# Optimization experiments

Hardware: AMD Instinct MI355X
Metric: run time of the kernel (lower is better)

Reference implementation:

```python
import jax, jax.numpy as jnp
import numpy as np

B, S, V, E, HL = 64, 30, 5000, 300, 256
TWOH = 2 * HL
KB, MAPD, MEMD, MLP, NCLS = 512, 512, 512, 1024, 32
L, T, NMOD, NOPS = 8, 9, 9, 6
IH, IW, CIN = 15, 10, 512 + 128


def setup_inputs():
    key = jax.random.key(0)
    ks = iter(jax.random.split(key, 64))
    g = lambda shape, s=0.05: jax.random.normal(next(ks), shape, jnp.float32) * s
    inp = {}
    inp['image'] = g((B, CIN, IH, IW), 1.0)
    inp['ques'] = jax.random.randint(next(ks), (B, S), 0, V)
    ql = jnp.sort(jax.random.randint(next(ks), (B,), 1, S + 1))[::-1]
    inp['q_len'] = ql.at[0].set(S)
    inp['embed_W'] = g((V, E))
    for d in ('f', 'b'):
        inp['lstm_Wi_' + d] = g((E, 4 * HL))
        inp['lstm_Wh_' + d] = g((HL, 4 * HL))
        inp['lstm_b_' + d] = jnp.zeros((4 * HL,), jnp.float32)
    inp['W1'] = g((T, TWOH, TWOH))
    inp['b_1'] = jnp.zeros((TWOH,), jnp.float32)
    inp['W2_w'] = g((2 * TWOH, TWOH)); inp['W2_b'] = jnp.zeros((TWOH,), jnp.float32)
    inp['W3'] = g((TWOH,))
    inp['c_0'] = g((TWOH,), 1.0)
    inp['Wmod'] = g((TWOH, NMOD))
    inp['ic1_w'] = g((KB, CIN)); inp['ic1_b'] = g((KB,), 1.0)
    inp['ic2_w'] = g((KB, KB)); inp['ic2_b'] = g((KB,), 1.0)
    inp['i2m_w'] = g((MAPD, KB)); inp['i2m_b'] = g((MAPD,), 1.0)
    inp['t2m_w'] = g((TWOH, MAPD)); inp['t2m_b'] = jnp.zeros((MAPD,), jnp.float32)
    inp['cell3_ow'] = g((4, NOPS), 1.0)
    inp['cell3_cw'] = g((4, MAPD)); inp['cell3_cb'] = jnp.zeros((4,), jnp.float32)
    inp['cell4_ow'] = g((2, NOPS), 1.0)
    inp['cell4_cw'] = g((2, MAPD)); inp['cell4_cb'] = jnp.zeros((2,), jnp.float32)
    inp['ans_ow'] = g((2, NOPS), 1.0)
    inp['ans_W'] = g((2, 2 * MAPD, MEMD)); inp['ans_b'] = jnp.zeros((2, MEMD), jnp.float32)
    inp['out1_w'] = g((TWOH + MEMD, MLP)); inp['out1_b'] = jnp.zeros((MLP,), jnp.float32)
    inp['out2_w'] = g((MLP, NCLS)); inp['out2_b'] = jnp.zeros((NCLS,), jnp.float32)
    return inp


def _conv1x1(x, w, b):
    return jnp.einsum('bchw,oc->bohw', x, w) + b[None, :, None, None]


def _lstm_dir(xW, Wh, mask, reverse):
    # xW: [S,B,4H], mask: [S,B,1] ; torch LSTM gate order i,f,g,o
    Bn, Hn = xW.shape[1], Wh.shape[0]
    def step(carry, inp):
        h, c = carry
        xw, m = inp
        z = xw + h @ Wh
        i, f, gg, o = jnp.split(z, 4, axis=-1)
        cn = jax.nn.sigmoid(f) * c + jax.nn.sigmoid(i) * jnp.tanh(gg)
        hn = jax.nn.sigmoid(o) * jnp.tanh(cn)
        return (jnp.where(m, hn, h), jnp.where(m, cn, c)), jnp.where(m, hn, 0.0)
    init = (jnp.zeros((Bn, Hn), xW.dtype), jnp.zeros((Bn, Hn), xW.dtype))
    (hF, _), outs = jax.lax.scan(step, init, (xW, mask), reverse=reverse)
    return hF, outs


def _mix3(ow, x, a, t):
    # soft op mixing (DARTS-style) for 3-input cells: x [B,D,H,W], a [B,H,W], t [B,D]
    w = jax.nn.softmax(ow)
    a4 = a[:, None]; t4 = t[:, :, None, None]
    ops = (x * t4, x + t4, x * a4, x * t4 * a4, x, a4 * t4)
    return jax.nn.elu(sum(w[k] * ops[k] for k in range(NOPS)))


def _mix4(ow, x, a1, a2, t):
    w = jax.nn.softmax(ow)
    a14 = a1[:, None]; a24 = a2[:, None]; t4 = t[:, :, None, None]
    ops = (x * t4, x + t4, x * a14, x * a24, x * a14 * a24, x * t4 * (a14 + a24))
    return jax.nn.elu(sum(w[k] * ops[k] for k in range(NOPS)))


def _forward(image, ques, q_len, embed_W, lstm_Wi_f, lstm_Wh_f, lstm_b_f, lstm_Wi_b, lstm_Wh_b, lstm_b_b, W1, b_1, W2_w, W2_b, W3, c_0, Wmod, ic1_w, ic1_b, ic2_w, ic2_b, i2m_w, i2m_b, t2m_w, t2m_b, cell3_ow, cell3_cw, cell3_cb, cell4_ow, cell4_cw, cell4_cb, ans_ow, ans_W, ans_b, out1_w, out1_b, out2_w, out2_b):
    # img_conv (1x1 conv -> ELU -> 1x1 conv)
    x = jax.nn.elu(_conv1x1(image, ic1_w, ic1_b))
    x = _conv1x1(x, ic2_w, ic2_b)
    Bn, _, Hh, Ww = x.shape
    Sn = ques.shape[1]
    # bi-LSTM over the (packed, i.e. masked) question
    emb = embed_W[ques]                                   # [B,S,E]
    mask = (jnp.arange(Sn)[None, :] < q_len[:, None])     # [B,S]
    mT = mask.T[:, :, None].astype(x.dtype) > 0           # [S,B,1] bool
    xWf = (emb @ lstm_Wi_f + lstm_b_f).transpose(1, 0, 2)
    xWb = (emb @ lstm_Wi_b + lstm_b_b).transpose(1, 0, 2)
    hF, oF = _lstm_dir(xWf, lstm_Wh_f, mT, False)
    hB, oB = _lstm_dir(xWb, lstm_Wh_b, mT, True)
    lstm_out = jnp.concatenate([oF, oB], -1).transpose(1, 0, 2)  # [B,S,2H], zero at pads
    q = jnp.concatenate([hF, hB], -1)                            # [B,2H]
    img_map = _conv1x1(x, i2m_w, i2m_b)                          # [B,MAP,H,W]
    stack = jnp.zeros((Bn, Hh, Ww, L), x.dtype)
    p = jnp.zeros((Bn, L), x.dtype).at[:, 0].set(1.0)
    mem = jnp.zeros((Bn, MEMD), x.dtype)
    c_prev = jnp.tile(c_0[None], (Bn, 1))
    e0 = jnp.zeros((L,), x.dtype).at[0].set(1.0)
    imp_loss = jnp.float32(0.0)
    read = lambda st, pp: jnp.einsum('bhwl,bl->bhw', st, pp)
    dec = lambda pp: jnp.concatenate([pp[:, 1:], jnp.zeros_like(pp[:, :1])], 1) + pp * e0
    for t in range(T):
        u = jnp.concatenate([q @ W1[t] + b_1, c_prev], 1) @ W2_w + W2_b  # [B,2H]
        wl = u @ Wmod                                                     # [B,9]
        ls = jax.nn.log_softmax(wl, axis=1)
        imp_loss = imp_loss - jnp.sum(jnp.exp(ls) * ls)
        w = jnp.exp(ls)
        attn = jax.nn.softmax(jnp.einsum('bsh,h->bs', lstm_out * u[:, None, :], W3), axis=1)
        c = jnp.einsum('bs,bsh->bh', attn, lstm_out)
        c_prev = c
        tmap = c @ t2m_w + t2m_b
        stacks, ps = [], []
        a_top = read(stack, p)     # attention at stack top
        # modules 0-3: overwrite at current pointer (pointer shift is commented out in source)
        for m in range(4):
            out = jnp.einsum('bdhw,d->bhw', _mix3(cell3_ow[m], img_map, a_top, tmap), cell3_cw[m]) + cell3_cb[m]
            pb = p[:, None, None, :]
            stacks.append(stack * (1.0 - pb) + out[..., None] * pb)
            ps.append(p)
        # modules 4-5: pop one (soft pointer decrement), then write
        p_dec = dec(p)
        a2 = read(stack, p_dec)
        for m in range(2):
            out = jnp.einsum('bdhw,d->bhw', _mix4(cell4_ow[m], img_map, a_top, a2, tmap), cell4_cw[m]) + cell4_cb[m]
            pb = p_dec[:, None, None, :]
            stacks.append(stack * (1.0 - pb) + out[..., None] * pb)
            ps.append(p_dec)
        # modules 6-7: answer cells -> memory update, stack untouched
        pooled6 = jnp.mean(_mix3(ans_ow[0], img_map, a_top, tmap), axis=(2, 3))
        mem6 = jnp.concatenate([pooled6, tmap], 1) @ ans_W[0] + ans_b[0]
        stacks.append(stack); ps.append(p)
        pooled7 = jnp.mean(_mix4(ans_ow[1], img_map, a_top, a2, tmap), axis=(2, 3))
        mem7 = jnp.concatenate([pooled7, tmap], 1) @ ans_W[1] + ans_b[1]
        stacks.append(stack); ps.append(p_dec)
        # module 8: NoOp
        stacks.append(stack); ps.append(p)
        # soft mixing over modules (the scatter-heavy part)
        stack = jnp.einsum('bm,bmhwl->bhwl', w, jnp.stack(stacks, 1))
        p = jnp.einsum('bm,bml->bl', w, jnp.stack(ps, 1))
        mem = w[:, 6:7] * mem6 + w[:, 7:8] * mem7 + (1.0 - w[:, 6:7] - w[:, 7:8]) * mem
    h1 = jax.nn.elu(jnp.concatenate([q, mem], 1) @ out1_w + out1_b)
    logits = h1 @ out2_w + out2_b
    return logits, imp_loss


def reference(image, ques, q_len, embed_W, lstm_Wi_f, lstm_Wh_f, lstm_b_f, lstm_Wi_b, lstm_Wh_b, lstm_b_b, W1, b_1, W2_w, W2_b, W3, c_0, Wmod, ic1_w, ic1_b, ic2_w, ic2_b, i2m_w, i2m_b, t2m_w, t2m_b, cell3_ow, cell3_cw, cell3_cb, cell4_ow, cell4_cw, cell4_cb, ans_ow, ans_W, ans_b, out1_w, out1_b, out2_w, out2_b):
    return _forward(image, ques, q_len, embed_W, lstm_Wi_f, lstm_Wh_f, lstm_b_f, lstm_Wi_b, lstm_Wh_b, lstm_b_b, W1, b_1, W2_w, W2_b, W3, c_0, Wmod, ic1_w, ic1_b, ic2_w, ic2_b, i2m_w, i2m_b, t2m_w, t2m_b, cell3_ow, cell3_cw, cell3_cb, cell4_ow, cell4_cw, cell4_cb, ans_ow, ans_W, ans_b, out1_w, out1_b, out2_w, out2_b)
```

## Files before the change

kernel.cpp:

```cpp
#include <hip/hip_runtime.h>
#include <hip/hip_fp16.h>
#include <math.h>

#define DEV __device__ __forceinline__

DEV float fexp(float x){ return __expf(x); }
DEV float elu_(float x){ return x > 0.f ? x : fexp(x) - 1.f; }
DEV float sigm_(float x){ return 1.f/(1.f + fexp(-x)); }
DEV float tanh_(float x){ float e = fexp(2.f*x); return 1.f - 2.f/(e + 1.f); }
DEV unsigned bf16r(float x){ unsigned u = __float_as_uint(x);
  return (u + 0x7fffu + ((u>>16)&1u)) >> 16; }
DEV float blo(unsigned u){ return __uint_as_float(u << 16); }
DEV float bhi(unsigned u){ return __uint_as_float(u & 0xffff0000u); }
DEV float bl(unsigned short u){ return __uint_as_float(((unsigned)u) << 16); }

using frag  = __attribute__((ext_vector_type(8))) short;
using fragh = __attribute__((ext_vector_type(8))) _Float16;
using f32x4 = __attribute__((ext_vector_type(4))) float;

DEV uint4 cload16w(const void* p){
  uint4 r;
  asm volatile("global_load_dwordx4 %0, %1, off sc0 sc1\n\ts_waitcnt vmcnt(0)"
               : "=v"(r) : "v"(p) : "memory");
  return r;
}
DEV uint4 cload16nw(const void* p){
  uint4 r;
  asm volatile("global_load_dwordx4 %0, %1, off sc0 sc1"
               : "=v"(r) : "v"(p) : "memory");
  return r;
}

DEV void d_packB(const float* __restrict__ W, short* __restrict__ Bp,
                 int KC, int Ng, int Ksrc, int N, int trans, int idx)
{
  if (idx >= KC*Ng*64) return;
  int lane = idx & 63;
  int g    = (idx >> 6) % Ng;
  int kc   = idx / (64*Ng);
  int n = g*16 + (lane & 15);
  int kb = kc*32 + ((lane >> 4) << 3);
  unsigned o[4];
#pragma unroll
  for (int jj = 0; jj < 4; ++jj) {
    int k0 = kb + 2*jj;
    float v0 = (k0   < Ksrc) ? (trans ? W[(size_t)n*Ksrc + k0]   : W[(size_t)(k0)*N + n])   : 0.f;
    float v1 = (k0+1 < Ksrc) ? (trans ? W[(size_t)n*Ksrc + k0+1] : W[(size_t)(k0+1)*N + n]) : 0.f;
    o[jj] = bf16r(v0) | (bf16r(v1) << 16);
  }
  *(uint4*)(Bp + (size_t)idx*8) = make_uint4(o[0], o[1], o[2], o[3]);
}

DEV void d_packImg(const float* __restrict__ image, short* __restrict__ Ap, int idx)
{
  int lane = idx & 63;
  int kc   = (idx >> 6) % 20;
  int mt   = idx / 1280;
  int row = mt*16 + (lane & 15);
  int b = row / 150, p = row % 150;
  int cb = kc*32 + ((lane >> 4) << 3);
  unsigned o[4];
#pragma unroll
  for (int jj = 0; jj < 4; ++jj) {
    float v0 = image[((size_t)b*640 + cb + 2*jj    )*150 + p];
    float v1 = image[((size_t)b*640 + cb + 2*jj + 1)*150 + p];
    o[jj] = bf16r(v0) | (bf16r(v1) << 16);
  }
  *(uint4*)(Ap + (size_t)idx*8) = make_uint4(o[0], o[1], o[2], o[3]);
}

DEV void d_packEmb(const float* __restrict__ embedW, const int* __restrict__ ques,
                   short* __restrict__ Ap, int idx)
{
  int lane = idx & 63;
  int kc   = (idx >> 6) % 10;
  int mt   = idx / 640;
  int row = mt*16 + (lane & 15);
  int q = ques[row];
  int kb = kc*32 + ((lane >> 4) << 3);
  unsigned o[4];
#pragma unroll
  for (int jj = 0; jj < 4; ++jj) {
    int k0 = kb + 2*jj;
    float v0 = (k0   < 300) ? embedW[(size_t)q*300 + k0]   : 0.f;
    float v1 = (k0+1 < 300) ? embedW[(size_t)q*300 + k0+1] : 0.f;
    o[jj] = bf16r(v0) | (bf16r(v1) << 16);
  }
  *(uint4*)(Ap + (size_t)idx*8) = make_uint4(o[0], o[1], o[2], o[3]);
}

__global__ __launch_bounds__(256)
void megapack_k(const float* __restrict__ c0, const float* __restrict__ c3ow,
                const float* __restrict__ c4ow, const float* __restrict__ aow,
                float* __restrict__ stack, float* __restrict__ pvecA,
                float* __restrict__ mem, float* __restrict__ cprev,
                float* __restrict__ swb, float* __restrict__ pl,
                const float* __restrict__ Whf, const float* __restrict__ Whb,
                unsigned* __restrict__ whT,
                float* __restrict__ hbufz, int* __restrict__ flagz,
                const float* __restrict__ ic1w, short* __restrict__ w1p,
                const float* __restrict__ ic2w, short* __restrict__ w2mp,
                const float* __restrict__ i2mw, short* __restrict__ w3mp,
                const float* __restrict__ Wif, short* __restrict__ wifp,
                const float* __restrict__ Wib, short* __restrict__ wibp,
                const float* __restrict__ image, short* __restrict__ imgP,
                const float* __restrict__ embedW, const int* __restrict__ ques,
                short* __restrict__ embp,
                const float* __restrict__ t2mw, unsigned* __restrict__ t2pp,
                const float* __restrict__ W2w, unsigned short* __restrict__ w2bp,
                const float* __restrict__ ansW, unsigned short* __restrict__ answp)
{
  const int bx = blockIdx.x, tid = threadIdx.x;
  if (bx < 320) {
    int idx = bx*256 + tid;
    int stride = 320*256;
    for (int i = idx; i < 64*150*8; i += stride) stack[i] = 0.f;
    for (int i = idx; i < 64*8;    i += stride) pvecA[i] = ((i & 7) == 0) ? 1.f : 0.f;
    for (int i = idx; i < 64*512;  i += stride) mem[i] = 0.f;
    for (int i = idx; i < 64*512;  i += stride) cprev[i] = c0[i & 511];
    for (int i = idx; i < 9*2*64*512; i += stride) pl[i] = 0.f;
    for (int i = idx; i < 32768;   i += stride) hbufz[i] = 0.f;
    if (idx < 256) flagz[idx] = 0;
    if (idx < 8) {
      const float* ow = (idx < 4) ? (c3ow + idx*6)
                      : (idx < 6) ? (c4ow + (idx-4)*6)
                                  : (aow  + (idx-6)*6);
      float mx = ow[0];
      for (int m = 1; m < 6; ++m) mx = fmaxf(mx, ow[m]);
      float e[6]; float s = 0.f;
      for (int m = 0; m < 6; ++m) { e[m] = fexp(ow[m]-mx); s += e[m]; }
      for (int m = 0; m < 6; ++m) swb[idx*6+m] = e[m]/s;
    }
  } else if (bx < 1344) {
    int idx = (bx-320)*256 + tid;
    int dd  = idx >> 17;
    int rem = idx & 131071;
    int kp  = rem >> 10;
    int zc  = rem & 1023;
    const float* Wh = dd ? Whb : Whf;
    __half2 hv = __floats2half2_rn(Wh[(size_t)(2*kp)*1024 + zc],
                                   Wh[(size_t)(2*kp+1)*1024 + zc]);
    whT[((size_t)dd << 17) + (zc << 7) + kp] = *(unsigned*)&hv;
  } else if (bx < 1504) {
    d_packB(ic1w, w1p, 20, 32, 640, 512, 1, (bx-1344)*256 + tid);
  } else if (bx < 1632) {
    d_packB(ic2w, w2mp, 16, 32, 512, 512, 1, (bx-1504)*256 + tid);
  } else if (bx < 1760) {
    d_packB(i2mw, w3mp, 16, 32, 512, 512, 1, (bx-1632)*256 + tid);
  } else if (bx < 1920) {
    d_packB(Wif, wifp, 10, 64, 300, 1024, 0, (bx-1760)*256 + tid);
  } else if (bx < 2080) {
    d_packB(Wib, wibp, 10, 64, 300, 1024, 0, (bx-1920)*256 + tid);
  } else if (bx < 5080) {
    d_packImg(image, imgP, (bx-2080)*256 + tid);
  } else if (bx < 5380) {
    d_packEmb(embedW, ques, embp, (bx-5080)*256 + tid);
  } else if (bx < 5892) {
    int idx = (bx-5380)*256 + tid;
    int k = idx >> 8, c = idx & 255;
    t2pp[idx] = bf16r(t2mw[(size_t)k*512 + c]) | (bf16r(t2mw[(size_t)k*512 + 256 + c]) << 16);
  } else if (bx < 7940) {
    int i = (bx-5892)*256 + tid;
    w2bp[i] = (unsigned short)bf16r(W2w[i]);
  } else {
    int i = (bx-7940)*256 + tid;
    answp[i] = (unsigned short)bf16r(ansW[i]);
  }
}

__global__ __launch_bounds__(256)
void gemmM_k(const short* __restrict__ ApA, const short* __restrict__ ApB,
             const short* __restrict__ BpA, const short* __restrict__ BpB,
             const float* __restrict__ biasA, const float* __restrict__ biasB,
             void* __restrict__ CoutA, void* __restrict__ CoutB,
             int KC, int Ng, int N, int mode, int act, int KCout)
{
  __shared__ float lds[4][16][68];
  const int z = blockIdx.z;
  const short* Ap = z ? ApB : ApA;
  const short* Bp = z ? BpB : BpA;
  const float* bias = z ? biasB : biasA;
  void* Cout = z ? CoutB : CoutA;
  const int tid = threadIdx.x, lane = tid & 63, w = tid >> 6;
// ... 145 lines not shown
              const float* __restrict__ c1bias, short* __restrict__ c1out)
{
  const int tid = threadIdx.x, lane = tid & 63, w = tid >> 6;
  __shared__ union {
    unsigned short Wl[65536];
    float lds[4][16][68];
  } sm;

  if (blockIdx.x >= 32) {
    const int bx2 = (int)blockIdx.x - 32;
    const int mt = (bx2 >> 3)*4 + w;
    const int ncol0 = (bx2 & 7)*64;
    const short* Abase = c1Ap + (((size_t)mt*20) << 9) + lane*8;
    const short* Bbase = c1Bp + (((size_t)(bx2 & 7)*4) << 9) + lane*8;
    f32x4 acc0 = {0.f,0.f,0.f,0.f}, acc1 = acc0, acc2 = acc0, acc3 = acc0;
#pragma unroll 2
    for (int kc = 0; kc < 20; ++kc) {
      frag a = *(const frag*)(Abase + ((size_t)kc << 9));
      const short* bk = Bbase + (((size_t)kc*32) << 9);
      frag b0 = *(const frag*)(bk);
      frag b1 = *(const frag*)(bk + 512);
      frag b2 = *(const frag*)(bk + 1024);
      frag b3 = *(const frag*)(bk + 1536);
      acc0 = __builtin_amdgcn_mfma_f32_16x16x32_bf16(a, b0, acc0, 0, 0, 0);
      acc1 = __builtin_amdgcn_mfma_f32_16x16x32_bf16(a, b1, acc1, 0, 0, 0);
      acc2 = __builtin_amdgcn_mfma_f32_16x16x32_bf16(a, b2, acc2, 0, 0, 0);
      acc3 = __builtin_amdgcn_mfma_f32_16x16x32_bf16(a, b3, acc3, 0, 0, 0);
    }
    {
      int colb = lane & 15, rowb = (lane >> 4)*4;
#pragma unroll
      for (int r = 0; r < 4; ++r) {
        sm.lds[w][rowb+r][ 0+colb] = acc0[r];
        sm.lds[w][rowb+r][16+colb] = acc1[r];
        sm.lds[w][rowb+r][32+colb] = acc2[r];
        sm.lds[w][rowb+r][48+colb] = acc3[r];
      }
    }
    __syncthreads();
    {
      int m = lane & 15, qb = (lane >> 4)*8;
#pragma unroll
      for (int h = 0; h < 2; ++h) {
        int nl = h*32 + qb;
        unsigned o[4];
#pragma unroll
        for (int jj = 0; jj < 4; ++jj) {
          float v0 = elu_(sm.lds[w][m][nl + 2*jj]     + c1bias[ncol0 + nl + 2*jj]);
          float v1 = elu_(sm.lds[w][m][nl + 2*jj + 1] + c1bias[ncol0 + nl + 2*jj + 1]);
          o[jj] = bf16r(v0) | (bf16r(v1) << 16);
        }
        *(uint4*)(c1out + (((size_t)mt*16 + (ncol0 >> 5) + h) << 9) + lane*8)
            = make_uint4(o[0], o[1], o[2], o[3]);
      }
    }
    return;
  }

  const int bx = blockIdx.x;
  const int d = bx & 1, g = (bx >> 1) & 3, n = bx >> 3;
  const int q = lane >> 4, cl = lane & 15;

#pragma unroll 4
  for (int rb = 0; rb < 32; ++rb) {
    int lcrow = rb*8 + (tid >> 5);
    int gt = lcrow >> 6, c = lcrow & 63;
    int zc = gt*256 + n*64 + c;
    uint4 v = *(const uint4*)(whT + (((size_t)d*1024 + zc) << 7) + ((tid & 31) << 2));
    int byteoff = (lcrow << 9) + ((((tid & 31) << 4)) ^ ((lcrow & 7) << 4));
    *(uint4*)((char*)sm.Wl + byteoff) = v;
  }

  const float* xW = d ? xWb : xWf;
  const int b   = g*16 + cl;
  const int c4  = w*16 + q*4;
  const int hc4 = n*64 + c4;
  const int len = qlen[b];
  float cst[4] = {0.f,0.f,0.f,0.f}, hst[4] = {0.f,0.f,0.f,0.f};
  int* flg = flags + ((d*4 + g) << 2);
  const int bofs = (cl & 7) << 4;
  __syncthreads();

  for (int ss = 0; ss < 30; ++ss) {
    const int s = d ? (29 - ss) : ss;
    const float* xr = xW + (size_t)b*30720 + (size_t)s*1024 + hc4;
    f32x4 xwv[4];
#pragma unroll
    for (int gt = 0; gt < 4; ++gt) xwv[gt] = *(const f32x4*)(xr + gt*256);

    if (ss > 0) {
      for (;;) {
        uint4 f4 = cload16w(flg);
        if ((int)f4.x >= ss && (int)f4.y >= ss &&
            (int)f4.z >= ss && (int)f4.w >= ss) break;
      }
      __builtin_amdgcn_sched_barrier(0);
    }
    const char* hbr = (const char*)(hbuf + ((size_t)(((ss & 1)*2 + d)*4 + g) << 9))
                    + (cl << 9) + (q << 4);
    union { uint4 u; fragh f; } hv[8];
#pragma unroll
    for (int ks = 0; ks < 8; ++ks) hv[ks].u = cload16nw(hbr + (ks << 6));
    asm volatile("s_waitcnt vmcnt(0)" ::: "memory");
    __builtin_amdgcn_sched_barrier(0);

    f32x4 acc0 = {0.f,0.f,0.f,0.f}, acc1 = acc0, acc2 = acc0, acc3 = acc0;
#pragma unroll
    for (int ks = 0; ks < 8; ++ks) {
      const int kb = ((ks << 6) + (q << 4)) ^ bofs;
      const char* wb = (const char*)sm.Wl + ((w*16 + cl) << 9) + kb;
      fragh a0 = *(const fragh*)(wb);
      fragh a1 = *(const fragh*)(wb + (64 << 9));
      fragh a2 = *(const fragh*)(wb + (128 << 9));
      fragh a3 = *(const fragh*)(wb + (192 << 9));
      acc0 = __builtin_amdgcn_mfma_f32_16x16x32_f16(a0, hv[ks].f, acc0, 0, 0, 0);
      acc1 = __builtin_amdgcn_mfma_f32_16x16x32_f16(a1, hv[ks].f, acc1, 0, 0, 0);
      acc2 = __builtin_amdgcn_mfma_f32_16x16x32_f16(a2, hv[ks].f, acc2, 0, 0, 0);
      acc3 = __builtin_amdgcn_mfma_f32_16x16x32_f16(a3, hv[ks].f, acc3, 0, 0, 0);
    }
    const bool m = s < len;
    f32x4 lo4;
    float hvv[4];
#pragma unroll
    for (int r = 0; r < 4; ++r) {
      float iv = acc0[r] + xwv[0][r];
      float fv = acc1[r] + xwv[1][r];
      float gv = acc2[r] + xwv[2][r];
      float o_ = acc3[r] + xwv[3][r];
      float cn = sigm_(fv)*cst[r] + sigm_(iv)*tanh_(gv);
      float hn = sigm_(o_)*tanh_(cn);
      float hk = m ? hn : hst[r];
      cst[r] = m ? cn : cst[r];
      hst[r] = hk;
      hvv[r] = hk;
      lo4[r] = m ? hn : 0.f;
    }
    unsigned long long* hbw = hbuf + ((size_t)((((ss & 1) ^ 1)*2 + d)*4 + g) << 9);
    union { unsigned long long u; __half2 h2[2]; } hp;
    hp.h2[0] = __floats2half2_rn(hvv[0], hvv[1]);
    hp.h2[1] = __floats2half2_rn(hvv[2], hvv[3]);
    __hip_atomic_store(hbw + cl*64 + (hc4 >> 2), hp.u,
                       __ATOMIC_RELAXED, __HIP_MEMORY_SCOPE_AGENT);
    *(f32x4*)(lstm_out + (((size_t)b*30 + s) << 9) + (d << 8) + hc4) = lo4;
    asm volatile("s_waitcnt vmcnt(0)" ::: "memory");
    __syncthreads();
    if (tid == 0)
      __hip_atomic_store(&flg[n], ss + 1, __ATOMIC_RELAXED, __HIP_MEMORY_SCOPE_AGENT);
  }
  *(f32x4*)(qout + ((size_t)b << 9) + (d << 8) + hc4) =
      f32x4{hst[0], hst[1], hst[2], hst[3]};
}

__global__ __launch_bounds__(1024)
void kcattn3_k(const float* __restrict__ u, const float* __restrict__ Wmod,
               const float* __restrict__ lstm_out, const float* __restrict__ W3,
               const unsigned* __restrict__ t2pp, const float* __restrict__ t2mb,
               float* __restrict__ woutAll, float* __restrict__ imp_part,
               float* __restrict__ cout, float* __restrict__ tmapv, int t)
{
  int b = blockIdx.x;
  int tid = threadIdx.x;
  int lane = tid & 63, wave = tid >> 6;
  __shared__ float ush[512];
  __shared__ float sC[512];
  __shared__ float cpart[512];
  __shared__ float tpart[4][512];
  __shared__ float wl[9];
  __shared__ float sc[32], at[32];
  if (tid < 512) ush[tid] = u[b*512 + tid];
  __syncthreads();
  for (int s = wave; s < 30; s += 16) {
    float acc = 0.f;
    const float* lo = lstm_out + ((size_t)b*30 + s)*512;
#pragma unroll
    for (int h = lane; h < 512; h += 64) acc += lo[h]*ush[h]*W3[h];
#pragma unroll
    for (int off = 32; off; off >>= 1) acc += __shfl_down(acc, off);
    if (lane == 0) sc[s] = acc;
  }
  if (wave < 9) {
    float acc = 0.f;
#pragma unroll
    for (int k = lane; k < 512; k += 64) acc += ush[k]*Wmod[k*9+wave];
#pragma unroll
    for (int off = 32; off; off >>= 1) acc += __shfl_down(acc, off);
    if (lane == 0) wl[wave] = acc;
  }
  __syncthreads();
  if (tid == 0) {
    float mx = wl[0];
    for (int m = 1; m < 9; ++m) mx = fmaxf(mx, wl[m]);
    float s = 0.f;
    for (int m = 0; m < 9; ++m) s += fexp(wl[m]-mx);
    float ls = logf(s);
    float ent = 0.f;
    for (int m = 0; m < 9; ++m) {
      float l = wl[m]-mx-ls;
      float w = fexp(l);
      woutAll[t*576 + b*9 + m] = w;
      ent -= w*l;
    }
    imp_part[t*64+b] = ent;
  }
  if (wave == 1) {
    float v = (lane < 30) ? sc[lane] : -3.4e38f;
    float mx = v;
#pragma unroll
    for (int off = 32; off; off >>= 1) mx = fmaxf(mx, __shfl_xor(mx, off));
    float e = (lane < 30) ? fexp(v-mx) : 0.f;
    float ssum = e;
#pragma unroll
    for (int off = 32; off; off >>= 1) ssum += __shfl_xor(ssum, off);
    if (lane < 30) at[lane] = e/ssum;
  }
  __syncthreads();
  {
    int h = tid & 511, seg = tid >> 9;
    float acc = 0.f;
    int s0 = seg ? 15 : 0, s1 = seg ? 30 : 15;
    for (int s = s0; s < s1; ++s) acc += at[s]*lstm_out[((size_t)b*30 + s)*512 + h];
    if (seg) cpart[h] = acc;
    __syncthreads();
    if (!seg) {
      float tot = acc + cpart[h];
      cout[b*512+h] = tot;
      sC[h] = tot;
    }
  }
  __syncthreads();
  {
    int c2 = tid & 255, ks = tid >> 8;
    float a0 = 0.f, a1 = 0.f;
    const unsigned* tp = t2pp + c2;
#pragma unroll 8
    for (int k = ks*128; k < ks*128 + 128; ++k) {
      float cv = sC[k];
      unsigned wv2 = tp[(size_t)k*256];
      a0 += cv*blo(wv2);
      a1 += cv*bhi(wv2);
    }
    tpart[ks][c2]       = a0;
    tpart[ks][256 + c2] = a1;
  }
  __syncthreads();
  if (tid < 512) {
    float v = tpart[0][tid] + tpart[1][tid] + tpart[2][tid] + tpart[3][tid];
    tmapv[b*512 + tid] = v + t2mb[tid];
  }
}

__global__ __launch_bounds__(256)
void modu_k(const unsigned short* __restrict__ imapB, const float* __restrict__ tmapv,
            float* __restrict__ stack, const float* __restrict__ pvecIn,
            float* __restrict__ pvecOut,
            const float* __restrict__ swb, const float* __restrict__ c3w,
            const float* __restrict__ c3b, const float* __restrict__ c4w,
            const float* __restrict__ c4b, const float* __restrict__ wmod,
            float* __restrict__ plt,
            const float* __restrict__ tmp1n, const float* __restrict__ cprevB,
            const unsigned short* __restrict__ w2bp, const float* __restrict__ W2b,
            float* __restrict__ ubuf, int do_u)
{
  __shared__ union {
    struct { float sT[512]; float pv[8], pd[8], wm[9]; float wpart[4][2][512]; } m;
    struct { __align__(16) float As[8][1024]; float part[4][8][64]; } u;
  } sm;
  int pb = blockIdx.y;
  int lane = threadIdx.x & 63, wave = threadIdx.x >> 6;
  if (pb == 19) {
    if (!do_u) return;
    const int x = blockIdx.x;
    const int r0 = (x >> 3) * 8, nc0 = (x & 7) * 64;
    for (int e4 = threadIdx.x; e4 < 2048; e4 += 256) {
      int r = e4 >> 8;
      int k4 = (e4 & 255) << 2;
      float4 v = (k4 < 512)
          ? *(const float4*)&tmp1n [(size_t)(r0+r)*512 + k4]
          : *(const float4*)&cprevB[(size_t)(r0+r)*512 + (k4 - 512)];
      *(float4*)&sm.u.As[r][k4] = v;
    }
    __syncthreads();
    const int k0 = wave * 256;
    const unsigned short* Bp = w2bp + (size_t)k0*512 + nc0 + lane;
    float acc[8] = {0,0,0,0,0,0,0,0};
#pragma unroll 4
    for (int kk = 0; kk < 256; ++kk) {
      float bv = bl(Bp[(size_t)kk*512]);
#pragma unroll
      for (int r = 0; r < 8; ++r) acc[r] += sm.u.As[r][k0+kk] * bv;
    }
#pragma unroll
    for (int r = 0; r < 8; ++r) sm.u.part[wave][r][lane] = acc[r];
    __syncthreads();
    {
      int r = threadIdx.x >> 6, c = lane;
#pragma unroll
      for (int p2 = 0; p2 < 2; ++p2) {
        int rr = r + p2*4;
        float s2 = sm.u.part[0][rr][c] + sm.u.part[1][rr][c]
                 + sm.u.part[2][rr][c] + sm.u.part[3][rr][c];
        ubuf[(size_t)(r0 + rr)*512 + nc0 + c] = s2 + W2b[nc0 + c];
      }
    }
    return;
  }
  int b = blockIdx.x;
  for (int j = threadIdx.x; j < 512; j += 256) sm.m.sT[j] = tmapv[b*512 + j];
  if (threadIdx.x < 8) sm.m.pv[threadIdx.x] = pvecIn[b*8+threadIdx.x];
  if (threadIdx.x >= 64 && threadIdx.x < 73) sm.m.wm[threadIdx.x-64] = wmod[b*9 + threadIdx.x-64];
  __syncthreads();
  if (threadIdx.x < 8) {
    int l = threadIdx.x;
    sm.m.pd[l] = (l < 7 ? sm.m.pv[l+1] : 0.f) + (l == 0 ? sm.m.pv[0] : 0.f);
  }
  __syncthreads();
  if (pb == 0 && threadIdx.x < 8) {
    int l = threadIdx.x;
    float WP = sm.m.wm[0]+sm.m.wm[1]+sm.m.wm[2]+sm.m.wm[3] + sm.m.wm[6] + sm.m.wm[8];
    float WD = sm.m.wm[4]+sm.m.wm[5] + sm.m.wm[7];
    pvecOut[b*8+l] = WP*sm.m.pv[l] + WD*sm.m.pd[l];
  }

  float W[8][6];
#pragma unroll
  for (int m = 0; m < 8; ++m)
#pragma unroll
    for (int i = 0; i < 6; ++i) W[m][i] = swb[m*6+i];
  float W03 = sm.m.wm[0]+sm.m.wm[1]+sm.m.wm[2]+sm.m.wm[3];
  float W45 = sm.m.wm[4]+sm.m.wm[5];

  float acc6[8], acc7[8];
#pragma unroll
  for (int i = 0; i < 8; ++i) { acc6[i] = 0.f; acc7[i] = 0.f; }

  for (int pi = 0; pi < 2; ++pi) {
    int p = pb*8 + wave*2 + pi;
    if (p < 150) {
      const float* st = stack + ((size_t)b*150 + p)*8;
      float a = 0.f, av2 = 0.f;
#pragma unroll
      for (int l = 0; l < 8; ++l) { float v = st[l]; a += v*sm.m.pv[l]; av2 += v*sm.m.pd[l]; }
      float part[6] = {0,0,0,0,0,0};
#pragma unroll 2
      for (int i = 0; i < 8; ++i) {
        int d = i*64 + lane;
        float x = bl(imapB[((size_t)b*150 + p)*512 + d]);
        float t = sm.m.sT[d];
#pragma unroll
        for (int m = 0; m < 4; ++m) {
          float c1 = W[m][0]*t + W[m][1] + W[m][4] + (W[m][2] + W[m][3]*t)*a;
          float c0 = W[m][1]*t + W[m][5]*t*a;
          part[m] += elu_(c1*x + c0) * c3w[m*512+d];
        }
#pragma unroll
        for (int m = 0; m < 2; ++m) {
          float c1 = W[4+m][0]*t + W[4+m][1] + W[4+m][2]*a + W[4+m][3]*av2
                   + W[4+m][4]*a*av2 + W[4+m][5]*t*(a+av2);
          part[4+m] += elu_(c1*x + W[4+m][1]*t) * c4w[m*512+d];
        }
        float c16 = W[6][0]*t + W[6][1] + W[6][4] + (W[6][2] + W[6][3]*t)*a;
        float c06 = W[6][1]*t + W[6][5]*t*a;
        acc6[i] += elu_(c16*x + c06);
        float c17 = W[7][0]*t + W[7][1] + W[7][2]*a + W[7][3]*av2
                  + W[7][4]*a*av2 + W[7][5]*t*(a+av2);
        acc7[i] += elu_(c17*x + W[7][1]*t);
      }
#pragma unroll
      for (int m = 0; m < 6; ++m) {
#pragma unroll
        for (int off = 32; off; off >>= 1) part[m] += __shfl_down(part[m], off);
        part[m] = __shfl(part[m], 0);
      }
      float r3  = sm.m.wm[0]*(part[0]+c3b[0]) + sm.m.wm[1]*(part[1]+c3b[1])
                + sm.m.wm[2]*(part[2]+c3b[2]) + sm.m.wm[3]*(part[3]+c3b[3]);
      float r45 = sm.m.wm[4]*(part[4]+c4b[0]) + sm.m.wm[5]*(part[5]+c4b[1]);
      if (lane < 8) {
        int l = lane;
        size_t idx = ((size_t)b*150 + p)*8 + l;
        stack[idx] = stack[idx]*(1.f - W03*sm.m.pv[l] - W45*sm.m.pd[l])
                   + sm.m.pv[l]*r3 + sm.m.pd[l]*r45;
      }
    }
  }
#pragma unroll
  for (int i = 0; i < 8; ++i) {
    sm.m.wpart[wave][0][i*64+lane] = acc6[i];
    sm.m.wpart[wave][1][i*64+lane] = acc7[i];
  }
  __syncthreads();
  for (int e = threadIdx.x; e < 1024; e += 256) {
    int which = e >> 9, d = e & 511;
    float s = sm.m.wpart[0][which][d] + sm.m.wpart[1][which][d]
            + sm.m.wpart[2][which][d] + sm.m.wpart[3][which][d];
    atomicAdd(&plt[(size_t)which*32768 + b*512 + d], s * (1.f/150.f));
  }
}

__global__ __launch_bounds__(512)
void ansall_k(const float* __restrict__ plt, const float* __restrict__ tmapv,
              const unsigned short* __restrict__ answp, const float* __restrict__ ansb,
              float* __restrict__ m67o)
{
  const int z = blockIdx.z;
  const int t = z >> 1, zz = z & 1;
  __shared__ __align__(16) float As[8][1024];
  __shared__ float part[8][8][64];
  const int tid = threadIdx.x;
  const int r0 = blockIdx.y*8;
  const int nc0 = blockIdx.x*64;
  const int lane = tid & 63, w = tid >> 6;

  for (int e4 = tid; e4 < 1024; e4 += 512) {
    int r = e4 >> 7, k4 = (e4 & 127) << 2;
    *(float4*)&As[r][k4]     = *(const float4*)&plt[(size_t)z*32768 + (size_t)(r0+r)*512 + k4];
    *(float4*)&As[r][512+k4] = *(const float4*)&tmapv[(size_t)t*32768 + (size_t)(r0+r)*512 + k4];
  }
  __syncthreads();
  {
    const unsigned short* Bp = answp + (size_t)zz*524288
                             + (size_t)(w*128)*512 + nc0 + lane;
    float acc[8] = {0,0,0,0,0,0,0,0};
    int k0 = w*128;
#pragma unroll 8
    for (int kk = 0; kk < 128; ++kk) {
      float bv = bl(Bp[(size_t)kk*512]);
#pragma unroll
      for (int r = 0; r < 8; ++r) acc[r] += As[r][k0+kk]*bv;
    }
#pragma unroll
    for (int r = 0; r < 8; ++r) part[w][r][lane] = acc[r];
  }
  __syncthreads();
  {
    int r = tid >> 6, c = tid & 63;
    float s = 0.f;
#pragma unroll
    for (int w2 = 0; w2 < 8; ++w2) s += part[w2][r][c];
    m67o[(size_t)z*32768 + (size_t)(r0+r)*512 + nc0 + c] = s + ansb[zz*512 + nc0 + c];
  }
}

__global__ __launch_bounds__(512)
void memfin_k(const float* __restrict__ woutAll, const float* __restrict__ m67t,
              float* __restrict__ memb)
{
  int b = blockIdx.x;
  int tid = threadIdx.x;
  __shared__ float w6s[9], w7s[9], coef[9];
  if (tid < 9)       w6s[tid] = woutAll[tid*576 + b*9 + 6];
  else if (tid < 18) w7s[tid-9] = woutAll[(tid-9)*576 + b*9 + 7];
  __syncthreads();
  if (tid == 0) {
    float c = 1.f;
    for (int t = 8; t >= 0; --t) { coef[t] = c; c *= (1.f - w6s[t] - w7s[t]); }
  }
  __syncthreads();
  float acc = 0.f;
#pragma unroll
  for (int t = 0; t < 9; ++t) {
    float m6 = m67t[(((size_t)t*2 + 0)*64 + b)*512 + tid];
    float m7 = m67t[(((size_t)t*2 + 1)*64 + b)*512 + tid];
    acc += coef[t]*(w6s[t]*m6 + w7s[t]*m7);
  }
  memb[b*512 + tid] = acc;
}

__global__ __launch_bounds__(256)
void imp_k(const float* __restrict__ part, float* __restrict__ out)
{
  int lane = threadIdx.x & 63, wave = threadIdx.x >> 6;
  float acc = 0.f;
  for (int i = threadIdx.x; i < 576; i += 256) acc += part[i];
#pragma unroll
  for (int off = 32; off; off >>= 1) acc += __shfl_down(acc, off);
  __shared__ float red[4];
  if (lane == 0) red[wave] = acc;
  __syncthreads();
  if (threadIdx.x == 0) out[0] = red[0]+red[1]+red[2]+red[3];
}

extern "C" void kernel_launch(void* const* d_in, const int* in_sizes, int n_in,
                              void* d_out, int out_size, void* d_ws, size_t ws_size,
                              hipStream_t stream)
{
  (void)in_sizes; (void)n_in; (void)out_size; (void)ws_size;
  const float* image = (const float*)d_in[0];
  const int*   ques  = (const int*)d_in[1];
  const int*   qlen  = (const int*)d_in[2];
  const float* embedW= (const float*)d_in[3];
  const float* Wi_f  = (const float*)d_in[4];
  const float* Wh_f  = (const float*)d_in[5];
  const float* b_f   = (const float*)d_in[6];
  const float* Wi_b  = (const float*)d_in[7];
  const float* Wh_b  = (const float*)d_in[8];
  const float* b_b   = (const float*)d_in[9];
  const float* W1    = (const float*)d_in[10];
  const float* b1    = (const float*)d_in[11];
  const float* W2w   = (const float*)d_in[12];
  const float* W2b   = (const float*)d_in[13];
  const float* W3    = (const float*)d_in[14];
  const float* c0    = (const float*)d_in[15];
  const float* Wmod  = (const float*)d_in[16];
  const float* ic1w  = (const float*)d_in[17];
  const float* ic1b  = (const float*)d_in[18];
  const float* ic2w  = (const float*)d_in[19];
  const float* ic2b  = (const float*)d_in[20];
  const float* i2mw  = (const float*)d_in[21];
  const float* i2mb  = (const float*)d_in[22];
  const float* t2mw  = (const float*)d_in[23];
  const float* t2mb  = (const float*)d_in[24];
  const float* c3ow  = (const float*)d_in[25];
  const float* c3cw  = (const float*)d_in[26];
  const float* c3cb  = (const float*)d_in[27];
  const float* c4ow  = (const float*)d_in[28];
  const float* c4cw  = (const float*)d_in[29];
  const float* c4cb  = (const float*)d_in[30];
  const float* aow   = (const float*)d_in[31];
  const float* ansW  = (const float*)d_in[32];
  const float* ansb  = (const float*)d_in[33];
  const float* o1w   = (const float*)d_in[34];
  const float* o1b   = (const float*)d_in[35];
  const float* o2w   = (const float*)d_in[36];
  const float* o2b   = (const float*)d_in[37];
  float* out = (float*)d_out;
  float* ws  = (float*)d_ws;

  size_t off = 0;
  auto alloc = [&](size_t n){ float* p = ws + off; off += n; return p; };
  short* imgP  = (short*)alloc(600ull*20*64*8/2);
  short* X1p   = (short*)alloc(600ull*16*64*8/2);
  short* X2p   = (short*)alloc(600ull*16*64*8/2);
  short* w1p   = (short*)alloc(20*32*64*8/2);
  short* w2mp  = (short*)alloc(16*32*64*8/2);
  short* w3mp  = (short*)alloc(16*32*64*8/2);
  short* wifp  = (short*)alloc(10*64*64*8/2);
  short* wibp  = (short*)alloc(10*64*64*8/2);
  short* embp  = (short*)alloc(120ull*10*64*8/2);
  unsigned short* imapB = (unsigned short*)alloc(9600ull*512/2);
  unsigned* t2pp = (unsigned*)alloc(512*256);
  unsigned short* w2bp  = (unsigned short*)alloc(524288/2);
  unsigned short* answp = (unsigned short*)alloc(1048576/2);
  float* xWfb  = alloc(64ull*30*1024);
  float* xWbb  = alloc(64ull*30*1024);
  float* lout  = alloc(64ull*30*512);
  float* qbuf  = alloc(64*512);
  float* stck  = alloc(64*150*8);
  float* pvecA = alloc(64*8);
  float* pvecB = alloc(64*8);
  float* memb  = alloc(64*512);
  float* cprev = alloc(64*512);
  float* tmp1a = alloc(9ull*64*512);
  float* ubuf  = alloc(64*512);
  float* wmwA  = alloc(9*64*9);
  float* impp  = alloc(9*64);
  float* swb   = alloc(48);
  float* pl    = alloc(9ull*2*64*512);
  float* m67t  = alloc(9ull*2*64*512);
  float* tmapv = alloc(9ull*64*512);
  float* h1b   = alloc(64*1024);
  unsigned* whT = (unsigned*)alloc(2ull*1024*128);
  float* hbufW  = alloc(32768);
  int*   flagsI = (int*)alloc(256);

  megapack_k<<<12036, 256, 0, stream>>>(
      c0, c3ow, c4ow, aow, stck, pvecA, memb, cprev, swb, pl,
      Wh_f, Wh_b, whT, hbufW, flagsI,
      ic1w, w1p, ic2w, w2mp, i2mw, w3mp, Wi_f, wifp, Wi_b, wibp,
      image, imgP, embedW, ques, embp, t2mw, t2pp,
      W2w, w2bp, ansW, answp);

  gemmM_k<<<dim3(16,30,2), 256, 0, stream>>>(embp, embp, wifp, wibp, b_f, b_b,
                                             xWfb, xWbb, 10, 64, 1024, 0, 0, 0);

  lstmc1_k<<<1232, 256, 0, stream>>>(xWfb, xWbb, whT, qlen,
                                     (unsigned long long*)hbufW, flagsI,
                                     lout, qbuf,
                                     imgP, w1p, ic1b, X1p);

  gemmM_k<<<dim3(8,150,1), 256, 0, stream>>>(X1p, X1p, w2mp, w2mp, ic2b, ic2b,
                                             X2p, X2p, 16, 32, 512, 1, 0, 16);
  gemmM_k<<<dim3(8,150,1), 256, 0, stream>>>(X2p, X2p, w3mp, w3mp, i2mb, i2mb,
                                             imapB, imapB, 16, 32, 512, 2, 0, 0);

  gemm64b_k<<<dim3(8,8,9), 512, 0, stream>>>(
      qbuf, 0, 9, (const float*)nullptr, 0,
      W1, 262144, b1, 0, tmp1a, 32768, 512, 0);
  gemm64b_k<<<dim3(8,8,1), 512, 0, stream>>>(
      tmp1a, 0, 9, cprev, 512, W2w, 0, W2b, 0, ubuf, 0, 512, 0);

  for (int t = 0; t < 9; ++t) {
    float* pvIn  = (t & 1) ? pvecB : pvecA;
    float* pvOut = (t & 1) ? pvecA : pvecB;
    kcattn3_k<<<64, 1024, 0, stream>>>(ubuf, Wmod, lout, W3, t2pp, t2mb,
                                       wmwA, impp, cprev,
                                       tmapv + (size_t)t*32768, t);
    modu_k<<<dim3(64,20), 256, 0, stream>>>(
        imapB, tmapv + (size_t)t*32768, stck, pvIn, pvOut, swb,
        c3cw, c3cb, c4cw, c4cb,
        wmwA + (size_t)t*576, pl + (size_t)t*65536,
        tmp1a + (size_t)(t < 8 ? t+1 : 0)*32768, cprev, w2bp, W2b, ubuf,
        (t < 8) ? 1 : 0);
  }

  ansall_k<<<dim3(8,8,18), 512, 0, stream>>>(pl, tmapv, answp, ansb, m67t);

  memfin_k<<<64, 512, 0, stream>>>(wmwA, m67t, memb);
  gemm64b_k<<<dim3(16,8,1), 512, 0, stream>>>(
      qbuf, 0, 9, memb, 512, o1w, 0, o1b, 0, h1b, 0, 1024, 1);
  gemm64b_k<<<dim3(1,8,1), 512, 0, stream>>>(
      h1b, 0, 10, (const float*)nullptr, 0, o2w, 0, o2b, 0, out, 0, 32, 0);
  imp_k<<<1, 256, 0, stream>>>(impp, out + 2048);
}
```

Measured before the change: 811.0 us.

## Fuse attention, u-update and module kernels into one software-pipelined step kernel

Merges the per-step attention kernel and the module/u-update kernel into a single 1024-thread launch. The module work for step t-1 runs alongside the attention for step t, and the u-GEMM blocks spin on per-batch flags for the fresh cprev instead of waiting on a kernel boundary. Module and u-GEMM blocks are widened to 16 waves with correspondingly split K and position ranges. This removes about half the launches and exposes cross-step overlap, in exchange for spin-wait synchronisation that assumes all blocks are co-resident, plus larger shared-memory unions.

```diff
diff --git a/kernel.cpp b/kernel.cpp
--- a/kernel.cpp
+++ b/kernel.cpp
@@ -29,6 +29,10 @@
   asm volatile("global_load_dwordx4 %0, %1, off sc0 sc1"
                : "=v"(r) : "v"(p) : "memory");
   return r;
+}
+DEV void cstore4(void* p, float v){
+  asm volatile("global_store_dword %0, %1, off sc0 sc1"
+               :: "v"(p), "v"(v) : "memory");
 }
 
 DEV void d_packB(const float* __restrict__ W, short* __restrict__ Bp,
@@ -480,170 +484,187 @@
 }
 
 __global__ __launch_bounds__(1024)
-void kcattn3_k(const float* __restrict__ u, const float* __restrict__ Wmod,
-               const float* __restrict__ lstm_out, const float* __restrict__ W3,
-               const unsigned* __restrict__ t2pp, const float* __restrict__ t2mb,
-               float* __restrict__ woutAll, float* __restrict__ imp_part,
-               float* __restrict__ cout, float* __restrict__ tmapv, int t)
-{
-  int b = blockIdx.x;
-  int tid = threadIdx.x;
-  int lane = tid & 63, wave = tid >> 6;
-  __shared__ float ush[512];
-  __shared__ float sC[512];
-  __shared__ float cpart[512];
-  __shared__ float tpart[4][512];
-  __shared__ float wl[9];
-  __shared__ float sc[32], at[32];
-  if (tid < 512) ush[tid] = u[b*512 + tid];
-  __syncthreads();
-  for (int s = wave; s < 30; s += 16) {
-    float acc = 0.f;
-    const float* lo = lstm_out + ((size_t)b*30 + s)*512;
-#pragma unroll
-    for (int h = lane; h < 512; h += 64) acc += lo[h]*ush[h]*W3[h];
-#pragma unroll
-    for (int off = 32; off; off >>= 1) acc += __shfl_down(acc, off);
-    if (lane == 0) sc[s] = acc;
-  }
-  if (wave < 9) {
-    float acc = 0.f;
-#pragma unroll
-    for (int k = lane; k < 512; k += 64) acc += ush[k]*Wmod[k*9+wave];
-#pragma unroll
-    for (int off = 32; off; off >>= 1) acc += __shfl_down(acc, off);
-    if (lane == 0) wl[wave] = acc;
-  }
-  __syncthreads();
-  if (tid == 0) {
-    float mx = wl[0];
-    for (int m = 1; m < 9; ++m) mx = fmaxf(mx, wl[m]);
-    float s = 0.f;
-    for (int m = 0; m < 9; ++m) s += fexp(wl[m]-mx);
-    float ls = logf(s);
-    float ent = 0.f;
-    for (int m = 0; m < 9; ++m) {
-      float l = wl[m]-mx-ls;
-      float w = fexp(l);
-      woutAll[t*576 + b*9 + m] = w;
-      ent -= w*l;
-    }
-    imp_part[t*64+b] = ent;
-  }
-  if (wave == 1) {
-    float v = (lane < 30) ? sc[lane] : -3.4e38f;
-    float mx = v;
-#pragma unroll
-    for (int off = 32; off; off >>= 1) mx = fmaxf(mx, __shfl_xor(mx, off));
-    float e = (lane < 30) ? fexp(v-mx) : 0.f;
-    float ssum = e;
-#pragma unroll
-    for (int off = 32; off; off >>= 1) ssum += __shfl_xor(ssum, off);
-    if (lane < 30) at[lane] = e/ssum;
-  }
-  __syncthreads();
-  {
-    int h = tid & 511, seg = tid >> 9;
-    float acc = 0.f;
-    int s0 = seg ? 15 : 0, s1 = seg ? 30 : 15;
-    for (int s = s0; s < s1; ++s) acc += at[s]*lstm_out[((size_t)b*30 + s)*512 + h];
-    if (seg) cpart[h] = acc;
+void step_k(const float* __restrict__ u, const float* __restrict__ Wmod,
+            const float* __restrict__ lstm_out, const float* __restrict__ W3,
+            const unsigned* __restrict__ t2pp, const float* __restrict__ t2mb,
+            float* __restrict__ woutAll, float* __restrict__ imp_part,
+            float* __restrict__ cprev, float* __restrict__ tmapv_k, int t,
+            const float* __restrict__ tmp1n, const unsigned short* __restrict__ w2bp,
+            const float* __restrict__ W2b, float* __restrict__ ubuf,
+            int* __restrict__ flags2, int do_u,
+            const unsigned short* __restrict__ imapB, const float* __restrict__ tmapv_m,
+            float* __restrict__ stack, const float* __restrict__ pvecIn,
+            float* __restrict__ pvecOut, const float* __restrict__ swb,
+            const float* __restrict__ c3w, const float* __restrict__ c3b,
+            const float* __restrict__ c4w, const float* __restrict__ c4b,
+            const float* __restrict__ wm_m, float* __restrict__ plt, int do_mod)
+{
+  const int tid = threadIdx.x;
+  const int lane = tid & 63, wave = tid >> 6;
+  __shared__ union {
+    struct {
+      float ush[512]; float sC[512]; float cpart[512]; float tpart[4][512];
+      float wl[9]; float sc[32], at[32];
+    } k;
+    struct {
+      __align__(16) float As[8][1024]; float part[16][8][64];
+    } uu;
+    struct {
+      float sT[512]; float pv[8], pd[8], wm[9]; float wpart[16][2][512];
+    } m;
+  } sm;
+
+  if (blockIdx.x < 64) {
+    if (t >= 9) return;
+    int b = blockIdx.x;
+    if (tid < 512) sm.k.ush[tid] = u[b*512 + tid];
     __syncthreads();
-    if (!seg) {
-      float tot = acc + cpart[h];
-      cout[b*512+h] = tot;
-      sC[h] = tot;
-    }
-  }
-  __syncthreads();
-  {
-    int c2 = tid & 255, ks = tid >> 8;
-    float a0 = 0.f, a1 = 0.f;
-    const unsigned* tp = t2pp + c2;
+    for (int s = wave; s < 30; s += 16) {
+      float acc = 0.f;
+      const float* lo = lstm_out + ((size_t)b*30 + s)*512;
+#pragma unroll
+      for (int h = lane; h < 512; h += 64) acc += lo[h]*sm.k.ush[h]*W3[h];
+#pragma unroll
+      for (int off = 32; off; off >>= 1) acc += __shfl_down(acc, off);
+      if (lane == 0) sm.k.sc[s] = acc;
+    }
+    if (wave < 9) {
+      float acc = 0.f;
+#pragma unroll
+      for (int k = lane; k < 512; k += 64) acc += sm.k.ush[k]*Wmod[k*9+wave];
+#pragma unroll
+      for (int off = 32; off; off >>= 1) acc += __shfl_down(acc, off);
+      if (lane == 0) sm.k.wl[wave] = acc;
+    }
+    __syncthreads();
+    if (tid == 0) {
+      float mx = sm.k.wl[0];
+      for (int m = 1; m < 9; ++m) mx = fmaxf(mx, sm.k.wl[m]);
+      float s = 0.f;
+      for (int m = 0; m < 9; ++m) s += fexp(sm.k.wl[m]-mx);
+      float ls = logf(s);
+      float ent = 0.f;
+      for (int m = 0; m < 9; ++m) {
+        float l = sm.k.wl[m]-mx-ls;
+        float w = fexp(l);
+        woutAll[t*576 + b*9 + m] = w;
+        ent -= w*l;
+      }
+      imp_part[t*64+b] = ent;
+    }
+    if (wave == 1) {
+      float v = (lane < 30) ? sm.k.sc[lane] : -3.4e38f;
+      float mx = v;
+#pragma unroll
+      for (int off = 32; off; off >>= 1) mx = fmaxf(mx, __shfl_xor(mx, off));
+      float e = (lane < 30) ? fexp(v-mx) : 0.f;
+      float ssum = e;
+#pragma unroll
+      for (int off = 32; off; off >>= 1) ssum += __shfl_xor(ssum, off);
+      if (lane < 30) sm.k.at[lane] = e/ssum;
+    }
+    __syncthreads();
+    {
+      int h = tid & 511, seg = tid >> 9;
+      float acc = 0.f;
+      int s0 = seg ? 15 : 0, s1 = seg ? 30 : 15;
+      for (int s = s0; s < s1; ++s) acc += sm.k.at[s]*lstm_out[((size_t)b*30 + s)*512 + h];
+      if (seg) sm.k.cpart[h] = acc;
+      __syncthreads();
+      if (!seg) {
+        float tot = acc + sm.k.cpart[h];
+        cstore4(&cprev[b*512+h], tot);
+        sm.k.sC[h] = tot;
+      }
+    }
+    asm volatile("s_waitcnt vmcnt(0)" ::: "memory");
+    __syncthreads();
+    if (tid == 0)
+      __hip_atomic_store(&flags2[b], t + 1, __ATOMIC_RELAXED, __HIP_MEMORY_SCOPE_AGENT);
+    {
+      int c2 = tid & 255, ks = tid >> 8;
+      float a0 = 0.f, a1 = 0.f;
+      const unsigned* tp = t2pp + c2;
 #pragma unroll 8
-    for (int k = ks*128; k < ks*128 + 128; ++k) {
-      float cv = sC[k];
-      unsigned wv2 = tp[(size_t)k*256];
-      a0 += cv*blo(wv2);
-      a1 += cv*bhi(wv2);
-    }
-    tpart[ks][c2]       = a0;
-    tpart[ks][256 + c2] = a1;
-  }
-  __syncthreads();
-  if (tid < 512) {
-    float v = tpart[0][tid] + tpart[1][tid] + tpart[2][tid] + tpart[3][tid];
-    tmapv[b*512 + tid] = v + t2mb[tid];
-  }
-}
-
-__global__ __launch_bounds__(256)
-void modu_k(const unsigned short* __restrict__ imapB, const float* __restrict__ tmapv,
-            float* __restrict__ stack, const float* __restrict__ pvecIn,
-            float* __restrict__ pvecOut,
-            const float* __restrict__ swb, const float* __restrict__ c3w,
-            const float* __restrict__ c3b, const float* __restrict__ c4w,
-            const float* __restrict__ c4b, const float* __restrict__ wmod,
-            float* __restrict__ plt,
-            const float* __restrict__ tmp1n, const float* __restrict__ cprevB,
-            const unsigned short* __restrict__ w2bp, const float* __restrict__ W2b,
-            float* __restrict__ ubuf, int do_u)
-{
-  __shared__ union {
-    struct { float sT[512]; float pv[8], pd[8], wm[9]; float wpart[4][2][512]; } m;
-    struct { __align__(16) float As[8][1024]; float part[4][8][64]; } u;
-  } sm;
-  int pb = blockIdx.y;
-  int lane = threadIdx.x & 63, wave = threadIdx.x >> 6;
-  if (pb == 19) {
+      for (int k = ks*128; k < ks*128 + 128; ++k) {
+        float cv = sm.k.sC[k];
+        unsigned wv2 = tp[(size_t)k*256];
+        a0 += cv*blo(wv2);
+        a1 += cv*bhi(wv2);
+      }
+      sm.k.tpart[ks][c2]       = a0;
+      sm.k.tpart[ks][256 + c2] = a1;
+    }
+    __syncthreads();
+    if (tid < 512) {
+      float v = sm.k.tpart[0][tid] + sm.k.tpart[1][tid]
+              + sm.k.tpart[2][tid] + sm.k.tpart[3][tid];
+      tmapv_k[b*512 + tid] = v + t2mb[tid];
+    }
+    return;
+  }
+
+  if (blockIdx.x < 128) {
     if (!do_u) return;
-    const int x = blockIdx.x;
+    const int x = (int)blockIdx.x - 64;
     const int r0 = (x >> 3) * 8, nc0 = (x & 7) * 64;
-    for (int e4 = threadIdx.x; e4 < 2048; e4 += 256) {
-      int r = e4 >> 8;
-      int k4 = (e4 & 255) << 2;
-      float4 v = (k4 < 512)
-          ? *(const float4*)&tmp1n [(size_t)(r0+r)*512 + k4]
-          : *(const float4*)&cprevB[(size_t)(r0+r)*512 + (k4 - 512)];
-      *(float4*)&sm.u.As[r][k4] = v;
+    {
+      int r = tid >> 7, k4 = (tid & 127) << 2;
+      *(float4*)&sm.uu.As[r][k4] = *(const float4*)&tmp1n[(size_t)(r0+r)*512 + k4];
+    }
+    if (tid == 0) {
+      for (;;) {
+        uint4 f0 = cload16w(flags2 + r0);
+        uint4 f1 = cload16w(flags2 + r0 + 4);
+        if ((int)f0.x > t && (int)f0.y > t && (int)f0.z > t && (int)f0.w > t &&
+            (int)f1.x > t && (int)f1.y > t && (int)f1.z > t && (int)f1.w > t) break;
+      }
     }
     __syncthreads();
-    const int k0 = wave * 256;
+    {
+      int r = tid >> 7, c4 = (tid & 127) << 2;
+      union { uint4 u4; float4 f4; } v;
+      v.u4 = cload16nw(&cprev[(size_t)(r0+r)*512 + c4]);
+      asm volatile("s_waitcnt vmcnt(0)" ::: "memory");
+      *(float4*)&sm.uu.As[r][512 + c4] = v.f4;
+    }
+    __syncthreads();
+    const int k0 = wave * 64;
     const unsigned short* Bp = w2bp + (size_t)k0*512 + nc0 + lane;
     float acc[8] = {0,0,0,0,0,0,0,0};
 #pragma unroll 4
-    for (int kk = 0; kk < 256; ++kk) {
+    for (int kk = 0; kk < 64; ++kk) {
       float bv = bl(Bp[(size_t)kk*512]);
 #pragma unroll
-      for (int r = 0; r < 8; ++r) acc[r] += sm.u.As[r][k0+kk] * bv;
-    }
-#pragma unroll
-    for (int r = 0; r < 8; ++r) sm.u.part[wave][r][lane] = acc[r];
+      for (int r = 0; r < 8; ++r) acc[r] += sm.uu.As[r][k0+kk] * bv;
+    }
+#pragma unroll
+    for (int r = 0; r < 8; ++r) sm.uu.part[wave][r][lane] = acc[r];
     __syncthreads();
-    {
-      int r = threadIdx.x >> 6, c = lane;
-#pragma unroll
-      for (int p2 = 0; p2 < 2; ++p2) {
-        int rr = r + p2*4;
-        float s2 = sm.u.part[0][rr][c] + sm.u.part[1][rr][c]
-                 + sm.u.part[2][rr][c] + sm.u.part[3][rr][c];
-        ubuf[(size_t)(r0 + rr)*512 + nc0 + c] = s2 + W2b[nc0 + c];
-      }
+    if (tid < 512) {
+      int r = tid >> 6, c = tid & 63;
+      float s2 = 0.f;
+#pragma unroll
+      for (int w2 = 0; w2 < 16; ++w2) s2 += sm.uu.part[w2][r][c];
+      ubuf[(size_t)(r0 + r)*512 + nc0 + c] = s2 + W2b[nc0 + c];
     }
     return;
   }
-  int b = blockIdx.x;
-  for (int j = threadIdx.x; j < 512; j += 256) sm.m.sT[j] = tmapv[b*512 + j];
-  if (threadIdx.x < 8) sm.m.pv[threadIdx.x] = pvecIn[b*8+threadIdx.x];
-  if (threadIdx.x >= 64 && threadIdx.x < 73) sm.m.wm[threadIdx.x-64] = wmod[b*9 + threadIdx.x-64];
-  __syncthreads();
-  if (threadIdx.x < 8) {
-    int l = threadIdx.x;
+
+  if (!do_mod) return;
+  const int mb = (int)blockIdx.x - 128;
+  const int b = mb & 63, pb = mb >> 6;
+  if (tid < 512) sm.m.sT[tid] = tmapv_m[b*512 + tid];
+  if (tid >= 512 && tid < 520) sm.m.pv[tid-512] = pvecIn[b*8 + (tid-512)];
+  if (tid >= 576 && tid < 585) sm.m.wm[tid-576] = wm_m[b*9 + (tid-576)];
+  __syncthreads();
+  if (tid < 8) {
+    int l = tid;
     sm.m.pd[l] = (l < 7 ? sm.m.pv[l+1] : 0.f) + (l == 0 ? sm.m.pv[0] : 0.f);
   }
   __syncthreads();
-  if (pb == 0 && threadIdx.x < 8) {
-    int l = threadIdx.x;
+  if (pb == 0 && tid < 8) {
+    int l = tid;
     float WP = sm.m.wm[0]+sm.m.wm[1]+sm.m.wm[2]+sm.m.wm[3] + sm.m.wm[6] + sm.m.wm[8];
     float WD = sm.m.wm[4]+sm.m.wm[5] + sm.m.wm[7];
     pvecOut[b*8+l] = WP*sm.m.pv[l] + WD*sm.m.pd[l];
@@ -662,7 +683,7 @@
   for (int i = 0; i < 8; ++i) { acc6[i] = 0.f; acc7[i] = 0.f; }
 
   for (int pi = 0; pi < 2; ++pi) {
-    int p = pb*8 + wave*2 + pi;
+    int p = pb*32 + wave*2 + pi;
     if (p < 150) {
       const float* st = stack + ((size_t)b*150 + p)*8;
       float a = 0.f, av2 = 0.f;
@@ -673,25 +694,25 @@
       for (int i = 0; i < 8; ++i) {
         int d = i*64 + lane;
         float x = bl(imapB[((size_t)b*150 + p)*512 + d]);
-        float t = sm.m.sT[d];
+        float t2 = sm.m.sT[d];
 #pragma unroll
         for (int m = 0; m < 4; ++m) {
-          float c1 = W[m][0]*t + W[m][1] + W[m][4] + (W[m][2] + W[m][3]*t)*a;
-          float c0 = W[m][1]*t + W[m][5]*t*a;
+          float c1 = W[m][0]*t2 + W[m][1] + W[m][4] + (W[m][2] + W[m][3]*t2)*a;
+          float c0 = W[m][1]*t2 + W[m][5]*t2*a;
           part[m] += elu_(c1*x + c0) * c3w[m*512+d];
         }
 #pragma unroll
         for (int m = 0; m < 2; ++m) {
-          float c1 = W[4+m][0]*t + W[4+m][1] + W[4+m][2]*a + W[4+m][3]*av2
-                   + W[4+m][4]*a*av2 + W[4+m][5]*t*(a+av2);
-          part[4+m] += elu_(c1*x + W[4+m][1]*t) * c4w[m*512+d];
+          float c1 = W[4+m][0]*t2 + W[4+m][1] + W[4+m][2]*a + W[4+m][3]*av2
+                   + W[4+m][4]*a*av2 + W[4+m][5]*t2*(a+av2);
+          part[4+m] += elu_(c1*x + W[4+m][1]*t2) * c4w[m*512+d];
         }
-        float c16 = W[6][0]*t + W[6][1] + W[6][4] + (W[6][2] + W[6][3]*t)*a;
-        float c06 = W[6][1]*t + W[6][5]*t*a;
+        float c16 = W[6][0]*t2 + W[6][1] + W[6][4] + (W[6][2] + W[6][3]*t2)*a;
+        float c06 = W[6][1]*t2 + W[6][5]*t2*a;
         acc6[i] += elu_(c16*x + c06);
-        float c17 = W[7][0]*t + W[7][1] + W[7][2]*a + W[7][3]*av2
-                  + W[7][4]*a*av2 + W[7][5]*t*(a+av2);
-        acc7[i] += elu_(c17*x + W[7][1]*t);
+        float c17 = W[7][0]*t2 + W[7][1] + W[7][2]*a + W[7][3]*av2
+                  + W[7][4]*a*av2 + W[7][5]*t2*(a+av2);
+        acc7[i] += elu_(c17*x + W[7][1]*t2);
       }
 #pragma unroll
       for (int m = 0; m < 6; ++m) {
@@ -716,10 +737,11 @@
     sm.m.wpart[wave][1][i*64+lane] = acc7[i];
   }
   __syncthreads();
-  for (int e = threadIdx.x; e < 1024; e += 256) {
-    int which = e >> 9, d = e & 511;
-    float s = sm.m.wpart[0][which][d] + sm.m.wpart[1][which][d]
-            + sm.m.wpart[2][which][d] + sm.m.wpart[3][which][d];
+  {
+    int which = tid >> 9, d = tid & 511;
+    float s = 0.f;
+#pragma unroll
+    for (int w2 = 0; w2 < 16; ++w2) s += sm.m.wpart[w2][which][d];
     atomicAdd(&plt[(size_t)which*32768 + b*512 + d], s * (1.f/150.f));
   }
 }
@@ -889,6 +911,7 @@
   unsigned* whT = (unsigned*)alloc(2ull*1024*128);
   float* hbufW  = alloc(32768);
   int*   flagsI = (int*)alloc(256);
+  int*   flags2 = flagsI + 64;
 
   megapack_k<<<12036, 256, 0, stream>>>(
       c0, c3ow, c4ow, aow, stck, pvecA, memb, cprev, swb, pl,
@@ -916,18 +939,20 @@
   gemm64b_k<<<dim3(8,8,1), 512, 0, stream>>>(
       tmp1a, 0, 9, cprev, 512, W2w, 0, W2b, 0, ubuf, 0, 512, 0);
 
-  for (int t = 0; t < 9; ++t) {
-    float* pvIn  = (t & 1) ? pvecB : pvecA;
-    float* pvOut = (t & 1) ? pvecA : pvecB;
-    kcattn3_k<<<64, 1024, 0, stream>>>(ubuf, Wmod, lout, W3, t2pp, t2mb,
-                                       wmwA, impp, cprev,
-                                       tmapv + (size_t)t*32768, t);
-    modu_k<<<dim3(64,20), 256, 0, stream>>>(
-        imapB, tmapv + (size_t)t*32768, stck, pvIn, pvOut, swb,
+  for (int t = 0; t <= 9; ++t) {
+    int tm = t - 1;
+    int tmc = (tm < 0) ? 0 : tm;
+    float* pvIn  = (tmc & 1) ? pvecB : pvecA;
+    float* pvOut = (tmc & 1) ? pvecA : pvecB;
+    step_k<<<448, 1024, 0, stream>>>(
+        ubuf, Wmod, lout, W3, t2pp, t2mb, wmwA, impp,
+        cprev, tmapv + (size_t)(t < 9 ? t : 0)*32768, t,
+        tmp1a + (size_t)(t < 8 ? t+1 : 0)*32768, w2bp, W2b, ubuf,
+        flags2, (t < 8) ? 1 : 0,
+        imapB, tmapv + (size_t)tmc*32768, stck, pvIn, pvOut, swb,
         c3cw, c3cb, c4cw, c4cb,
-        wmwA + (size_t)t*576, pl + (size_t)t*65536,
-        tmp1a + (size_t)(t < 8 ? t+1 : 0)*32768, cprev, w2bp, W2b, ubuf,
-        (t < 8) ? 1 : 0);
+        wmwA + (size_t)tmc*576, pl + (size_t)tmc*65536,
+        (t > 0) ? 1 : 0);
   }
 
   ansall_k<<<dim3(8,8,18), 512, 0, stream>>>(pl, tmapv, answp, ansb, m67t);
```

Result: faster. 787.0 us (-3.0%).
